# Kernel tuning notes

Hardware: AMD Instinct MI355X
Metric: run time of the kernel (lower is better)

The kernel has to match this reference:

```python
import jax, jax.numpy as jnp
import numpy as np

P, Q = 5, 4
C_IN, C_OUT = 256, 256


def setup_inputs() -> dict:
    key = jax.random.key(0)
    kx, kwp, kbp, kwq = jax.random.split(key, 4)
    x = jax.random.normal(kx, (32, C_IN, 56, 56), dtype=jnp.float32)
    # 1x1 conv weights: convp_i -> Wp[i-1] of shape [O, C]; only convp_1 has bias.
    Wp = jax.random.normal(kwp, (P, C_OUT, C_IN), dtype=jnp.float32) * (1.0 / np.sqrt(C_IN))
    bp = jax.random.normal(kbp, (C_OUT,), dtype=jnp.float32) * 0.01
    Wq = jax.random.normal(kwq, (Q, C_OUT, C_IN), dtype=jnp.float32) * (1.0 / np.sqrt(C_IN))
    return {"x": x, "Wp": Wp, "bp": bp, "Wq": Wq}


def reference(x, Wp, bp, Wq):
    # Build powers x**1 .. x**max(P,Q) via incremental multiply (same math as x**i).
    pmax = max(P, Q)
    pows = [x]
    for _ in range(pmax - 1):
        pows.append(pows[-1] * x)
    Xs = jnp.stack(pows, axis=0)  # [pmax, B, C, H, W]
    # Each 1x1 conv is a pointwise channel-mixing GEMM; sum over orders p/q.
    sum_p = jnp.einsum('pbchw,poc->bohw', Xs[:P], Wp) + bp[None, :, None, None]
    sum_q = jnp.einsum('qbchw,qoc->bohw', Xs[:Q], Wq)
    return sum_p / (1.0 + jnp.abs(sum_q))
```

## Files before the change

kernel.cpp:

```cpp
#include <hip/hip_runtime.h>


typedef __attribute__((ext_vector_type(8))) short bf16x8;
typedef __attribute__((ext_vector_type(4))) float f32x4;
typedef __attribute__((ext_vector_type(2))) float f32x2;

#define CIN    256
#define HW3    3136
#define MTOT   100352
#define KTOT   1280
#define WPLANE (512 * 1280)

__device__ __forceinline__ unsigned short f2bf(float f) {
    union { float f; unsigned int u; } cv; cv.f = f;
    unsigned int u = cv.u;
    return (unsigned short)((u + 0x7FFFu + ((u >> 16) & 1u)) >> 16);
}
__device__ __forceinline__ float bf2f(unsigned short h) {
    union { unsigned int u; float f; } cv; cv.u = ((unsigned int)h) << 16;
    return cv.f;
}

__global__ void pack_w_kernel(const float* __restrict__ Wp,
                              const float* __restrict__ Wq,
                              unsigned short* __restrict__ Whi,
                              unsigned short* __restrict__ Wlo) {
    int idx = blockIdx.x * 256 + threadIdx.x;
    int n = idx / KTOT;
    int k = idx - n * KTOT;
    int p = k >> 8, c = k & 255;
    int o = ((n >> 5) << 4) + (n & 15);
    int isq = (n >> 4) & 1;
    float v;
    if (isq) v = (p < 4) ? Wq[((size_t)p * 256 + o) * 256 + c] : 0.0f;
    else     v = Wp[((size_t)p * 256 + o) * 256 + c];
    unsigned short h = f2bf(v);
    Whi[idx] = h;
    Wlo[idx] = f2bf(v - bf2f(h));
}

__device__ __forceinline__ unsigned int fbits(float f) {
    union { float f; unsigned int u; } c; c.f = f; return c.u;
}
__device__ __forceinline__ float ubits(unsigned int u) {
    union { unsigned int u; float f; } c; c.u = u; return c.f;
}

__device__ __forceinline__ bf16x8 pack_hi8v(const f32x2* p) {
    union { unsigned int w[4]; bf16x8 h; } r;
#pragma unroll
    for (int j = 0; j < 4; ++j)
        r.w[j] = __builtin_amdgcn_perm(fbits(p[j].y), fbits(p[j].x), 0x07060302);
    return r.h;
}
__device__ __forceinline__ void resid4v(const f32x2* v, f32x2* l) {
#pragma unroll
    for (int j = 0; j < 4; ++j) {
        f32x2 h;
        h.x = ubits(fbits(v[j].x) & 0xFFFF0000u);
        h.y = ubits(fbits(v[j].y) & 0xFFFF0000u);
        l[j] = v[j] - h;
    }
}

__global__ __launch_bounds__(256, 3) void kanv_gemm(
    const float* __restrict__ x,
    const unsigned short* __restrict__ Whi,
    const unsigned short* __restrict__ Wlo,
    const float* __restrict__ bp,
    float* __restrict__ out)
{
    __shared__ __align__(16) char sB[9 * 4096];

    const int tid  = threadIdx.x;
    const int lane = tid & 63;
    const int wave = tid >> 6;
    const int col  = lane & 15;
    const int quad = lane >> 4;

    const int bid  = blockIdx.x;
    const int orig = (bid & 7) * 784 + (bid >> 3);
    const int nt = orig & 7;
    const int mt = orig >> 3;
    const int m0 = mt * 128 + wave * 32;

    const float* xc[2];
#pragma unroll
    for (int mi = 0; mi < 2; ++mi) {
        int m  = m0 + mi * 16 + col;
        int bb = m / HW3, hw = m - bb * HW3;
        xc[mi] = x + ((size_t)bb * CIN + quad * 8) * HW3 + hw;
    }

    const int voff = (nt * 64 + wave * 16 + col) * 2560 + quad * 16;

    const int rbase = quad * 256 + col * 16;

    f32x4 acc[2][4];
#pragma unroll
    for (int mi = 0; mi < 2; ++mi)
#pragma unroll
        for (int ni = 0; ni < 4; ++ni)
            acc[mi][ni] = (f32x4){0.f, 0.f, 0.f, 0.f};

    f32x2 xvA[2][4], xvB[2][4];

#pragma unroll
    for (int mi = 0; mi < 2; ++mi) {
#pragma unroll
        for (int j = 0; j < 4; ++j) {
            f32x2 v;
            v.x = xc[mi][(size_t)(2 * j) * HW3];
            v.y = xc[mi][(size_t)(2 * j + 1) * HW3];
            xvA[mi][j] = v;
        }
        xc[mi] += (size_t)32 * HW3;
    }

    auto body = [&](int g, f32x2 (&XV)[2][4], f32x2 (&XN)[2][4]) {
        __syncthreads();

#pragma unroll
        for (int s = 0; s < 9; ++s) {
            const unsigned short* plane = (s < 5) ? Whi : Wlo;
            const int p = (s < 5) ? s : (s - 4);
            const char* srcb = (const char*)plane + (size_t)((p * 256 + g * 32) * 2);
            __builtin_amdgcn_global_load_lds(
                (const __attribute__((address_space(1))) void*)(srcb + voff),
                (__attribute__((address_space(3))) void*)(sB + s * 4096 + wave * 1024),
                16, 0, 0);
        }
        __syncthreads();

        if (g < 7) {
#pragma unroll
            for (int mi = 0; mi < 2; ++mi) {
#pragma unroll
                for (int j = 0; j < 4; ++j) {
                    f32x2 v;
                    v.x = xc[mi][(size_t)(2 * j) * HW3];
                    v.y = xc[mi][(size_t)(2 * j + 1) * HW3];
                    XN[mi][j] = v;
                }
                xc[mi] += (size_t)32 * HW3;
            }
        }

        f32x2 pw[2][4];
        bf16x8 ahC[2], alC[2];
#pragma unroll
        for (int mi = 0; mi < 2; ++mi) {
            ahC[mi] = pack_hi8v(XV[mi]);
#pragma unroll
            for (int j = 0; j < 4; ++j)
                pw[mi][j] = XV[mi][j] * XV[mi][j];
        }
#pragma unroll
        for (int p = 0; p < 5; ++p) {
            bf16x8 ahN[2], alN[2];
            if (p < 4) {
#pragma unroll
                for (int mi = 0; mi < 2; ++mi) {
                    ahN[mi] = pack_hi8v(pw[mi]);
                    f32x2 lo[4];
                    resid4v(pw[mi], lo);
                    alN[mi] = pack_hi8v(lo);
                }
                if (p < 3) {
#pragma unroll
                    for (int mi = 0; mi < 2; ++mi)
#pragma unroll
                        for (int j = 0; j < 4; ++j)
                            pw[mi][j] *= XV[mi][j];
                }
            }
            const char* sb_p = sB + p * 4096 + rbase;
#pragma unroll
            for (int ni = 0; ni < 4; ++ni) {
                if (p == 4 && (ni & 1)) continue;
                bf16x8 bh = *(const bf16x8*)(sb_p + ni * 1024);
#pragma unroll
                for (int mi = 0; mi < 2; ++mi)
                    acc[mi][ni] = __builtin_amdgcn_mfma_f32_16x16x32_bf16(ahC[mi], bh, acc[mi][ni], 0, 0, 0);
                if (p > 0) {
                    bf16x8 bl = *(const bf16x8*)(sB + (p + 4) * 4096 + rbase + ni * 1024);
#pragma unroll
                    for (int mi = 0; mi < 2; ++mi) {
                        acc[mi][ni] = __builtin_amdgcn_mfma_f32_16x16x32_bf16(alC[mi], bh, acc[mi][ni], 0, 0, 0);
                        acc[mi][ni] = __builtin_amdgcn_mfma_f32_16x16x32_bf16(ahC[mi], bl, acc[mi][ni], 0, 0, 0);
                    }
                }
            }
#pragma unroll
            for (int mi = 0; mi < 2; ++mi) { ahC[mi] = ahN[mi]; alC[mi] = alN[mi]; }
        }
    };

    for (int gg = 0; gg < 4; ++gg) {
        body(2 * gg,     xvA, xvB);
        body(2 * gg + 1, xvB, xvA);
    }

#pragma unroll
    for (int j = 0; j < 2; ++j) {
        const int o = (nt * 2 + j) * 16 + col;
        const float bias = bp[o];
#pragma unroll
        for (int mi = 0; mi < 2; ++mi) {
            f32x4 sp = acc[mi][2 * j];
            f32x4 sq = acc[mi][2 * j + 1];
            const int mrow = m0 + mi * 16 + quad * 4;
            const int b2  = mrow / HW3;
            const int hw2 = mrow - b2 * HW3;
            float4 v;
            v.x = (sp[0] + bias) / (1.0f + fabsf(sq[0]));
            v.y = (sp[1] + bias) / (1.0f + fabsf(sq[1]));
            v.z = (sp[2] + bias) / (1.0f + fabsf(sq[2]));
            v.w = (sp[3] + bias) / (1.0f + fabsf(sq[3]));
            *(float4*)&out[((size_t)b2 * 256 + o) * HW3 + hw2] = v;
        }
    }
}

extern "C" void kernel_launch(void* const* d_in, const int* in_sizes, int n_in,
                              void* d_out, int out_size, void* d_ws, size_t ws_size,
                              hipStream_t stream) {
    const float* x  = (const float*)d_in[0];
    const float* Wp = (const float*)d_in[1];
    const float* bp = (const float*)d_in[2];
    const float* Wq = (const float*)d_in[3];
    float* out = (float*)d_out;
    unsigned short* Whi = (unsigned short*)d_ws;
    unsigned short* Wlo = Whi + WPLANE;

    pack_w_kernel<<<WPLANE / 256, 256, 0, stream>>>(Wp, Wq, Whi, Wlo);
    kanv_gemm<<<(MTOT / 128) * 8, 256, 0, stream>>>(x, Whi, Wlo, bp, out);
}
```

Before: 463.6 us.

## Double-buffer hi weights in LDS and load lo weights directly from global

Hi-part weight tiles now go into two LDS buffers, so the next K-group is staged while the current one is computed, and each iteration needs one barrier instead of two. The p=4 hi slice, which only has P rows, is staged by half the waves. Lo-part weights skip LDS and are read straight from global memory into registers one order ahead, and the next x values are prefetched partway through the order loop. This hides load latency and halves LDS traffic, at the cost of more registers and more global-memory (cache) traffic for the lo weights.

```diff
diff --git a/kernel.cpp b/kernel.cpp
--- a/kernel.cpp
+++ b/kernel.cpp
@@ -10,6 +10,7 @@
 #define MTOT   100352
 #define KTOT   1280
 #define WPLANE (512 * 1280)
+#define BUFSZ  18432
 
 __device__ __forceinline__ unsigned short f2bf(float f) {
     union { float f; unsigned int u; } cv; cv.f = f;
@@ -70,7 +71,7 @@
     const float* __restrict__ bp,
     float* __restrict__ out)
 {
-    __shared__ __align__(16) char sB[9 * 4096];
+    __shared__ __align__(16) char sB[2 * BUFSZ];
 
     const int tid  = threadIdx.x;
     const int lane = tid & 63;
@@ -92,7 +93,15 @@
         xc[mi] = x + ((size_t)bb * CIN + quad * 8) * HW3 + hw;
     }
 
-    const int voff = (nt * 64 + wave * 16 + col) * 2560 + quad * 16;
+    const unsigned short* wl[4];
+#pragma unroll
+    for (int ni = 0; ni < 4; ++ni) {
+        int n = nt * 64 + ni * 16 + col;
+        wl[ni] = Wlo + (size_t)n * KTOT + quad * 8;
+    }
+
+    const int voff  = (nt * 64 + wave * 16 + col) * 2560 + quad * 16;
+    const int voff4 = (nt * 64 + (wave >> 1) * 32 + col) * 2560 + quad * 16;
 
     const int rbase = quad * 256 + col * 16;
 
@@ -103,8 +112,26 @@
         for (int ni = 0; ni < 4; ++ni)
             acc[mi][ni] = (f32x4){0.f, 0.f, 0.f, 0.f};
 
-    f32x2 xvA[2][4], xvB[2][4];
-
+    auto stage = [&](int bs, int g) {
+        char* dstb = sB + bs * BUFSZ;
+        const char* whib = (const char*)Whi;
+#pragma unroll
+        for (int s = 0; s < 4; ++s) {
+            __builtin_amdgcn_global_load_lds(
+                (const __attribute__((address_space(1))) void*)(whib + (size_t)((s * 256 + g * 32) * 2) + voff),
+                (__attribute__((address_space(3))) void*)(dstb + s * 4096 + wave * 1024),
+                16, 0, 0);
+        }
+        if ((wave & 1) == 0) {
+            __builtin_amdgcn_global_load_lds(
+                (const __attribute__((address_space(1))) void*)(whib + (size_t)((4 * 256 + g * 32) * 2) + voff4),
+                (__attribute__((address_space(3))) void*)(dstb + 16384 + (wave >> 1) * 1024),
+                16, 0, 0);
+        }
+    };
+
+    stage(0, 0);
+    f32x2 XV[2][4];
 #pragma unroll
     for (int mi = 0; mi < 2; ++mi) {
 #pragma unroll
@@ -112,39 +139,22 @@
             f32x2 v;
             v.x = xc[mi][(size_t)(2 * j) * HW3];
             v.y = xc[mi][(size_t)(2 * j + 1) * HW3];
-            xvA[mi][j] = v;
+            XV[mi][j] = v;
         }
         xc[mi] += (size_t)32 * HW3;
     }
-
-    auto body = [&](int g, f32x2 (&XV)[2][4], f32x2 (&XN)[2][4]) {
-        __syncthreads();
-
-#pragma unroll
-        for (int s = 0; s < 9; ++s) {
-            const unsigned short* plane = (s < 5) ? Whi : Wlo;
-            const int p = (s < 5) ? s : (s - 4);
-            const char* srcb = (const char*)plane + (size_t)((p * 256 + g * 32) * 2);
-            __builtin_amdgcn_global_load_lds(
-                (const __attribute__((address_space(1))) void*)(srcb + voff),
-                (__attribute__((address_space(3))) void*)(sB + s * 4096 + wave * 1024),
-                16, 0, 0);
-        }
-        __syncthreads();
-
-        if (g < 7) {
-#pragma unroll
-            for (int mi = 0; mi < 2; ++mi) {
-#pragma unroll
-                for (int j = 0; j < 4; ++j) {
-                    f32x2 v;
-                    v.x = xc[mi][(size_t)(2 * j) * HW3];
-                    v.y = xc[mi][(size_t)(2 * j + 1) * HW3];
-                    XN[mi][j] = v;
-                }
-                xc[mi] += (size_t)32 * HW3;
-            }
-        }
+    __syncthreads();
+
+    int bufo = 0;
+    for (int g = 0; g < 8; ++g) {
+        const char* cbuf = sB + bufo * BUFSZ;
+
+        if (g < 7) stage(bufo ^ 1, g + 1);
+
+        bf16x8 blC[4];
+#pragma unroll
+        for (int ni = 0; ni < 4; ++ni)
+            blC[ni] = *(const bf16x8*)(wl[ni] + 1 * 256 + g * 32);
 
         f32x2 pw[2][4];
         bf16x8 ahC[2], alC[2];
@@ -155,9 +165,10 @@
             for (int j = 0; j < 4; ++j)
                 pw[mi][j] = XV[mi][j] * XV[mi][j];
         }
+
 #pragma unroll
         for (int p = 0; p < 5; ++p) {
-            bf16x8 ahN[2], alN[2];
+            bf16x8 ahN[2], alN[2], blN[4];
             if (p < 4) {
 #pragma unroll
                 for (int mi = 0; mi < 2; ++mi) {
@@ -174,31 +185,56 @@
                             pw[mi][j] *= XV[mi][j];
                 }
             }
-            const char* sb_p = sB + p * 4096 + rbase;
+            if (p >= 1 && p < 4) {
+#pragma unroll
+                for (int ni = 0; ni < 4; ++ni)
+                    blN[ni] = *(const bf16x8*)(wl[ni] + (p + 1) * 256 + g * 32);
+            }
+            if (p == 3 && g < 7) {
+#pragma unroll
+                for (int mi = 0; mi < 2; ++mi) {
+#pragma unroll
+                    for (int j = 0; j < 4; ++j) {
+                        f32x2 v;
+                        v.x = xc[mi][(size_t)(2 * j) * HW3];
+                        v.y = xc[mi][(size_t)(2 * j + 1) * HW3];
+                        XV[mi][j] = v;
+                    }
+                    xc[mi] += (size_t)32 * HW3;
+                }
+            }
+
 #pragma unroll
             for (int ni = 0; ni < 4; ++ni) {
                 if (p == 4 && (ni & 1)) continue;
-                bf16x8 bh = *(const bf16x8*)(sb_p + ni * 1024);
+                const char* ba = (p < 4)
+                    ? (cbuf + p * 4096 + ni * 1024 + rbase)
+                    : (cbuf + 16384 + (ni >> 1) * 1024 + rbase);
+                bf16x8 bh = *(const bf16x8*)ba;
 #pragma unroll
                 for (int mi = 0; mi < 2; ++mi)
                     acc[mi][ni] = __builtin_amdgcn_mfma_f32_16x16x32_bf16(ahC[mi], bh, acc[mi][ni], 0, 0, 0);
                 if (p > 0) {
-                    bf16x8 bl = *(const bf16x8*)(sB + (p + 4) * 4096 + rbase + ni * 1024);
 #pragma unroll
                     for (int mi = 0; mi < 2; ++mi) {
                         acc[mi][ni] = __builtin_amdgcn_mfma_f32_16x16x32_bf16(alC[mi], bh, acc[mi][ni], 0, 0, 0);
-                        acc[mi][ni] = __builtin_amdgcn_mfma_f32_16x16x32_bf16(ahC[mi], bl, acc[mi][ni], 0, 0, 0);
+                        acc[mi][ni] = __builtin_amdgcn_mfma_f32_16x16x32_bf16(ahC[mi], blC[ni], acc[mi][ni], 0, 0, 0);
                     }
                 }
             }
-#pragma unroll
-            for (int mi = 0; mi < 2; ++mi) { ahC[mi] = ahN[mi]; alC[mi] = alN[mi]; }
-        }
-    };
-
-    for (int gg = 0; gg < 4; ++gg) {
-        body(2 * gg,     xvA, xvB);
-        body(2 * gg + 1, xvB, xvA);
+
+            if (p < 4) {
+#pragma unroll
+                for (int mi = 0; mi < 2; ++mi) { ahC[mi] = ahN[mi]; alC[mi] = alN[mi]; }
+                if (p >= 1) {
+#pragma unroll
+                    for (int ni = 0; ni < 4; ++ni) blC[ni] = blN[ni];
+                }
+            }
+        }
+
+        __syncthreads();
+        bufo ^= 1;
     }
 
 #pragma unroll
```

Result: slower. 594.5 us (+28.2%).
